# Performance work log

Hardware: AMD Instinct MI355X
Metric: run time of the kernel (lower is better)

Reference implementation:

```python
import jax, jax.numpy as jnp
import numpy as np
import math

B, H, S, F = 2, 16, 2048, 128

def setup_inputs() -> dict:
    key = jax.random.key(0)
    ks = jax.random.split(key, 7)
    scale = 1.0 / math.sqrt(F)
    x = jax.random.normal(ks[0], (B, H, S, F), dtype=jnp.float32)
    # torch nn.Linear weight is [out, in]; stacked per head -> [H, out, in]
    Wq = jax.random.uniform(ks[1], (H, F, F), jnp.float32, -scale, scale)
    Wk = jax.random.uniform(ks[2], (H, F, F), jnp.float32, -scale, scale)
    Wv = jax.random.uniform(ks[3], (H, F, F), jnp.float32, -scale, scale)
    bq = jax.random.uniform(ks[4], (H, F), jnp.float32, -scale, scale)
    bk = jax.random.uniform(ks[5], (H, F), jnp.float32, -scale, scale)
    bv = jax.random.uniform(ks[6], (H, F), jnp.float32, -scale, scale)
    return {"x": x, "Wq": Wq, "Wk": Wk, "Wv": Wv, "bq": bq, "bk": bk, "bv": bv}

def reference(x, Wq, Wk, Wv, bq, bk, bv):
    # Per-head linear projections (y = x @ W.T + b), batched over heads via einsum
    q = jnp.einsum('bhsf,hef->bhse', x, Wq) + bq[None, :, None, :]
    k = jnp.einsum('bhsf,hef->bhse', x, Wk) + bk[None, :, None, :]
    v = jnp.einsum('bhsf,hef->bhse', x, Wv) + bv[None, :, None, :]
    # Scores [B,H,S,S]
    scores = jnp.einsum('bhqe,bhke->bhqk', q, k)
    # Causal mask (strict upper triangle set to -inf) applied BEFORE scaling,
    # matching the original (dividing -inf by sqrt(F) keeps it -inf)
    causal = jnp.triu(jnp.ones((S, S), dtype=bool), k=1)
    scores = jnp.where(causal[None, None], -jnp.inf, scores)
    scores = scores / jnp.sqrt(jnp.float32(x.shape[-1]))
    weights = jax.nn.softmax(scores, axis=-1)
    return jnp.einsum('bhqk,bhke->bhqe', weights, v)
```

## Files before the change

kernel.cpp:

```cpp
#include <hip/hip_runtime.h>
#include <hip/hip_bf16.h>

#define SLEN 2048
#define FDIM 128
#define NH   16
#define NBH  32
#define QBLK 64
#define KVB  64
#define NQT  (SLEN / QBLK)

typedef __attribute__((ext_vector_type(8)))  __bf16 bf16x8;
typedef __attribute__((ext_vector_type(8)))  short  s16x8;
typedef __attribute__((ext_vector_type(4)))  short  s16x4;
typedef __attribute__((ext_vector_type(4)))  float  f32x4;
typedef __attribute__((ext_vector_type(16))) float  f32x16;
typedef __attribute__((ext_vector_type(4)))  int    i32x4;

__device__ __forceinline__ unsigned short f2bf_u(float f) {
    union { float f; unsigned u; } t;
    t.f = f;
    unsigned r = t.u + 0x7FFFu + ((t.u >> 16) & 1u);
    return (unsigned short)(r >> 16);
}
__device__ __forceinline__ short f2bf(float f) { return (short)f2bf_u(f); }
__device__ __forceinline__ unsigned pack2(float a, float b) {
    return (unsigned)f2bf_u(a) | ((unsigned)f2bf_u(b) << 16);
}

__device__ __forceinline__ float ex2(float x) {
    float r;
    asm volatile("v_exp_f32 %0, %1" : "=v"(r) : "v"(x));
    return r;
}

__device__ __forceinline__ void gld16(const void* g, void* l) {
    __builtin_amdgcn_global_load_lds(
        (const __attribute__((address_space(1))) void*)g,
        (__attribute__((address_space(3))) void*)l, 16, 0, 0);
}

__global__ __launch_bounds__(256, 2) void qkv_proj(
    const float* __restrict__ x,
    const float* __restrict__ Wq, const float* __restrict__ Wk, const float* __restrict__ Wv,
    const float* __restrict__ bq, const float* __restrict__ bk, const float* __restrict__ bv,
    short* __restrict__ Q, short* __restrict__ K, short* __restrict__ Vt)
{
    const int zi = blockIdx.z;
    const int bh = blockIdx.y;
    const int h  = bh & (NH - 1);
    const int st = blockIdx.x;

    const float* W    = (zi == 0) ? Wq : (zi == 1) ? Wk : Wv;
    const float* bias = (zi == 0) ? bq : (zi == 1) ? bk : bv;
    W    += (size_t)h * FDIM * FDIM;
    bias += h * FDIM;
    const float* xg = x + ((size_t)bh * SLEN + st * 64) * FDIM;

    __shared__ __align__(16) short lx[64][136];
    __shared__ __align__(16) short lw[128][136];

    const int t = threadIdx.x;
    {
        int r = t >> 4, c = (t & 15) * 8;
        #pragma unroll
        for (int it = 0; it < 4; ++it) {
            const float* src = &xg[(size_t)(r + it * 16) * FDIM + c];
            f32x4 a = *(const f32x4*)&src[0];
            f32x4 b = *(const f32x4*)&src[4];
            s16x8 o;
            #pragma unroll
            for (int j = 0; j < 4; ++j) { o[j] = f2bf(a[j]); o[4 + j] = f2bf(b[j]); }
            *(s16x8*)&lx[r + it * 16][c] = o;
        }
        #pragma unroll
        for (int it = 0; it < 8; ++it) {
            const float* src = &W[(size_t)(r + it * 16) * FDIM + c];
            f32x4 a = *(const f32x4*)&src[0];
            f32x4 b = *(const f32x4*)&src[4];
            s16x8 o;
            #pragma unroll
            for (int j = 0; j < 4; ++j) { o[j] = f2bf(a[j]); o[4 + j] = f2bf(b[j]); }
            *(s16x8*)&lw[r + it * 16][c] = o;
        }
    }
    __syncthreads();

    const int wid = t >> 6, lane = t & 63;
    const int wr = (wid >> 1) * 32;
    const int wc = (wid & 1) * 64;
    const int lr = lane & 15, lk = (lane >> 4) * 8, hi4 = (lane >> 4) * 4;

    f32x4 acc[2][4] = {};
    #pragma unroll
    for (int ks = 0; ks < 4; ++ks) {
        int kb = ks * 32 + lk;
        bf16x8 a[2], b[4];
        #pragma unroll
        for (int m = 0; m < 2; ++m) a[m] = *(const bf16x8*)&lx[wr + m * 16 + lr][kb];
        #pragma unroll
        for (int n = 0; n < 4; ++n) b[n] = *(const bf16x8*)&lw[wc + n * 16 + lr][kb];
        #pragma unroll
        for (int m = 0; m < 2; ++m)
            #pragma unroll
            for (int n = 0; n < 4; ++n)
                acc[m][n] = __builtin_amdgcn_mfma_f32_16x16x32_bf16(a[m], b[n], acc[m][n], 0, 0, 0);
    }

    if (zi == 0) {
        short* og = Q + ((size_t)bh * SLEN + st * 64) * FDIM;
        const float sc = 0.12751744526f;
        #pragma unroll
        for (int n = 0; n < 4; ++n) {
            int col = wc + n * 16 + lr;
            float bb = bias[col];
            #pragma unroll
            for (int m = 0; m < 2; ++m) {
                int r0 = wr + m * 16 + hi4;
                #pragma unroll
                for (int j = 0; j < 4; ++j)
                    og[(size_t)(r0 + j) * FDIM + col] = f2bf((acc[m][n][j] + bb) * sc);
            }
        }
    } else if (zi == 1) {
        short* og = K + (size_t)bh * SLEN * FDIM;
        #pragma unroll
        for (int n = 0; n < 4; ++n) {
            int col = wc + n * 16 + lr;
            float bb = bias[col];
            #pragma unroll
            for (int m = 0; m < 2; ++m) {
                int s0 = st * 64 + wr + m * 16 + hi4;
                #pragma unroll
                for (int j = 0; j < 4; ++j) {
                    int s = s0 + j;
                    int idx = (s * FDIM + col) ^ ((s & 15) << 3);
                    og[idx] = f2bf(acc[m][n][j] + bb);
                }
            }
        }
    } else {
        short* ogT = Vt + (size_t)bh * SLEN * FDIM;
        const int hp = (hi4 == 4) ? 8 : (hi4 == 8) ? 4 : hi4;
        #pragma unroll
        for (int n = 0; n < 4; ++n) {
            int col = wc + n * 16 + lr;
            float bb = bias[col];
            const int cb  = col >> 5, qlp = col & 31;
            #pragma unroll
            for (int m = 0; m < 2; ++m) {
                const int kb16 = wr + m * 16;
                const int hs_  = kb16 >> 5;
                const int s2_  = (kb16 >> 4) & 1;
                const int hi2_ = hp >> 3;
                const int j0   = hp & 7;
                s16x4 w;
                #pragma unroll
                for (int j = 0; j < 4; ++j) w[j] = f2bf(acc[m][n][j] + bb);
                size_t addr = (size_t)st * 8192 + hs_ * 4096 + cb * 1024
                            + s2_ * 512 + (hi2_ * 32 + qlp) * 8 + j0;
                *(s16x4*)&ogT[addr] = w;
            }
        }
    }
}

__global__ __launch_bounds__(256, 2) void attn_fwd(
    const short* __restrict__ Qg, const short* __restrict__ Kg,
    const short* __restrict__ vTg, float* __restrict__ out)
{
    __shared__ __align__(16) char smem[34816];
    float* obuf = (float*)smem;
    float* mlb  = (float*)(smem + 33792);

    const int bid = blockIdx.x;
    const int qt  = (NQT - 1) - (bid >> 5);
    const int bh  = bid & 31;

    const int t = threadIdx.x, wid = t >> 6, lane = t & 63;
    const int ql  = lane & 31;
    const int hi2 = lane >> 5;
    const int qb  = wid & 1;
    const int hs  = wid >> 1;
    const size_t base = (size_t)bh * SLEN * FDIM;

    const char*  kgb = (const char*)(Kg + base);
    const short* vgb = vTg + base + hs * 4096 + (size_t)lane * 8;

    bf16x8 qf[8];
    {
        const short* qp = Qg + base + (size_t)(qt * QBLK + qb * 32 + ql) * FDIM;
        #pragma unroll
        for (int ks = 0; ks < 8; ++ks) qf[ks] = *(const bf16x8*)&qp[ks * 16 + hi2 * 8];
    }

    f32x16 oacc[4] = {};
    float m_run = -1e30f, l_run = 0.f;

    #define STAGE(ktile, buf) do {                                               \
        const char* kt_ = kgb + (size_t)(ktile) * 16384;                         \
        _Pragma("unroll")                                                        \
        for (int i_ = 0; i_ < 4; ++i_)                                           \
            gld16(kt_ + wid * 4096 + i_ * 1024 + lane * 16,                      \
                  smem + (buf) * 16384 + wid * 4096 + i_ * 1024);                \
    } while (0)

    STAGE(0, 0);
    __syncthreads();

    const int nkt = qt + 1;
    int cur = 0;
    const int kswz = (ql & 15) << 3;

    for (int kt = 0; kt < nkt; ++kt) {
        bf16x8 vfr[8];
        {
            const short* vb_ = vgb + (size_t)kt * 8192;
            #pragma unroll
            for (int cb = 0; cb < 4; ++cb) {
                vfr[cb * 2 + 0] = *(const bf16x8*)&vb_[cb * 1024];
                vfr[cb * 2 + 1] = *(const bf16x8*)&vb_[cb * 1024 + 512];
            }
        }
        if (kt + 1 < nkt) STAGE(kt + 1, cur ^ 1);

        const char* kbuf = smem + cur * 16384;

        const int Rrow = hs * 32 + ql;
        f32x16 sfr = {};
        __builtin_amdgcn_s_setprio(1);
        #pragma unroll
        for (int ks = 0; ks < 8; ++ks) {
            bf16x8 kf = *(const bf16x8*)(kbuf + (size_t)(((Rrow * 128 + ks * 16 + hi2 * 8) ^ kswz) * 2));
            sfr = __builtin_amdgcn_mfma_f32_32x32x16_bf16(kf, qf[ks], sfr, 0, 0, 0);
        }
        __builtin_amdgcn_s_setprio(0);

        if (kt == qt) {
            if (hs > qb) {
                #pragma unroll
                for (int r = 0; r < 16; ++r) sfr[r] = -__builtin_inff();
            } else if (hs == qb) {
                #pragma unroll
                for (int r = 0; r < 16; ++r) {
                    int kl = (r & 3) + 8 * (r >> 2) + 4 * hi2;
                    if (kl > ql) sfr[r] = -__builtin_inff();
                }
            }
        }

        float a0 = fmaxf(fmaxf(sfr[0],  sfr[1]),  sfr[2]);
        float a1 = fmaxf(fmaxf(sfr[3],  sfr[4]),  sfr[5]);
        float a2 = fmaxf(fmaxf(sfr[6],  sfr[7]),  sfr[8]);
        float a3 = fmaxf(fmaxf(sfr[9],  sfr[10]), sfr[11]);
        float a4 = fmaxf(fmaxf(sfr[12], sfr[13]), sfr[14]);
        float b0 = fmaxf(fmaxf(a0, a1), a2);
        float b1 = fmaxf(fmaxf(a3, a4), sfr[15]);
        float rm = fmaxf(b0, b1);
        rm = fmaxf(rm, __shfl_xor(rm, 32));
        if (!__all(rm <= m_run)) {
            float mnew = fmaxf(m_run, rm);
            float fac  = ex2(m_run - mnew);
            l_run *= fac;
            #pragma unroll
            for (int cb = 0; cb < 4; ++cb) oacc[cb] *= fac;
            m_run = mnew;
        }
        float pe[16];
        #pragma unroll
        for (int r = 0; r < 16; ++r) pe[r] = ex2(sfr[r] - m_run);
        float s0 = (pe[0] + pe[1]) + (pe[2] + pe[3]);
        float s1 = (pe[4] + pe[5]) + (pe[6] + pe[7]);
        float s2 = (pe[8] + pe[9]) + (pe[10] + pe[11]);
        float s3 = (pe[12] + pe[13]) + (pe[14] + pe[15]);
        float ssum = (s0 + s1) + (s2 + s3);
        l_run += ssum + __shfl_xor(ssum, 32);

        bf16x8 pf[2];
        #pragma unroll
        for (int s2_ = 0; s2_ < 2; ++s2_) {
            const int b = s2_ * 8;
            union { unsigned u[4]; bf16x8 v; } w;
            w.u[0] = pack2(pe[b + 0], pe[b + 1]);
            w.u[1] = pack2(pe[b + 2], pe[b + 3]);
            w.u[2] = pack2(pe[b + 4], pe[b + 5]);
            w.u[3] = pack2(pe[b + 6], pe[b + 7]);
            pf[s2_] = w.v;
        }

        __builtin_amdgcn_s_setprio(1);
        #pragma unroll
        for (int cb = 0; cb < 4; ++cb) {
            #pragma unroll
            for (int s2_ = 0; s2_ < 2; ++s2_)
                oacc[cb] = __builtin_amdgcn_mfma_f32_32x32x16_bf16(vfr[cb * 2 + s2_], pf[s2_], oacc[cb], 0, 0, 0);
        }
        __builtin_amdgcn_s_setprio(0);

        __syncthreads();
        cur ^= 1;
    }
    #undef STAGE

    if (lane < 32) {
        mlb[(wid * 32 + ql) * 2 + 0] = m_run;
        mlb[(wid * 32 + ql) * 2 + 1] = l_run;
    }
    if (hs == 1) {
        #pragma unroll
        for (int cb = 0; cb < 4; ++cb)
            #pragma unroll
            for (int r = 0; r < 16; ++r) {
                int e = cb * 32 + (r & 3) + 8 * (r >> 2) + 4 * hi2;
                obuf[(qb * 32 + ql) * 132 + e] = oacc[cb][r];
            }
    }
    __syncthreads();
    if (hs == 0) {
        float m2 = mlb[((wid + 2) * 32 + ql) * 2 + 0];
        float l2 = mlb[((wid + 2) * 32 + ql) * 2 + 1];
        float M  = fmaxf(m_run, m2);
        float a  = ex2(m_run - M);
        float b2 = ex2(m2 - M);
        float inv = 1.f / (l_run * a + l2 * b2);
        float* orow = out + base + (size_t)(qt * QBLK + qb * 32 + ql) * FDIM;
        #pragma unroll
        for (int cb = 0; cb < 4; ++cb)
            #pragma unroll
            for (int r = 0; r < 16; ++r) {
                int e = cb * 32 + (r & 3) + 8 * (r >> 2) + 4 * hi2;
                orow[e] = (oacc[cb][r] * a + obuf[(qb * 32 + ql) * 132 + e] * b2) * inv;
            }
    }
}

extern "C" void kernel_launch(void* const* d_in, const int* in_sizes, int n_in,
                              void* d_out, int out_size, void* d_ws, size_t ws_size,
                              hipStream_t stream) {
    (void)in_sizes; (void)n_in; (void)out_size; (void)ws_size;
    const float* x  = (const float*)d_in[0];
    const float* Wq = (const float*)d_in[1];
    const float* Wk = (const float*)d_in[2];
    const float* Wv = (const float*)d_in[3];
    const float* bq = (const float*)d_in[4];
    const float* bk = (const float*)d_in[5];
    const float* bv = (const float*)d_in[6];

    const size_t elems = (size_t)NBH * SLEN * FDIM;
    short* Q  = (short*)d_ws;
    short* K  = Q + elems;
    short* Vt = K + elems;

    qkv_proj<<<dim3(SLEN / 64, NBH, 3), 256, 0, stream>>>(x, Wq, Wk, Wv, bq, bk, bv, Q, K, Vt);
    attn_fwd<<<dim3(NQT * NBH), 256, 0, stream>>>(Q, K, Vt, (float*)d_out);
}
```

Baseline: 93.30 us.

## Fuse QKV projections per tile, pre-convert weights, reorder attention tiles

```diff
diff --git a/kernel.cpp b/kernel.cpp
--- a/kernel.cpp
+++ b/kernel.cpp
@@ -23,8 +23,11 @@
     return (unsigned short)(r >> 16);
 }
 __device__ __forceinline__ short f2bf(float f) { return (short)f2bf_u(f); }
-__device__ __forceinline__ unsigned pack2(float a, float b) {
-    return (unsigned)f2bf_u(a) | ((unsigned)f2bf_u(b) << 16);
+
+__device__ __forceinline__ unsigned cvt_pk_bf16(float lo, float hi) {
+    unsigned r;
+    asm("v_cvt_pk_bf16_f32 %0, %1, %2" : "=v"(r) : "v"(lo), "v"(hi));
+    return r;
 }
 
 __device__ __forceinline__ float ex2(float x) {
@@ -39,27 +42,56 @@
         (__attribute__((address_space(3))) void*)l, 16, 0, 0);
 }
 
-__global__ __launch_bounds__(256, 2) void qkv_proj(
-    const float* __restrict__ x,
-    const float* __restrict__ Wq, const float* __restrict__ Wk, const float* __restrict__ Wv,
+__global__ __launch_bounds__(256, 4) void wconv(
+    const float* __restrict__ Wq, const float* __restrict__ Wk,
+    const float* __restrict__ Wv, short* __restrict__ Wb)
+{
+    const int bid = blockIdx.x;
+    const int z = bid >> 6, rem = bid & 63;
+    const int h = rem >> 2, qd = rem & 3;
+    const float* Wm = ((z == 0) ? Wq : (z == 1) ? Wk : Wv) + (size_t)h * 16384;
+    short* O = Wb + ((size_t)z * NH + h) * 16384;
+    const int t = threadIdx.x;
+    #pragma unroll
+    for (int it = 0; it < 2; ++it) {
+        int idx = qd * 4096 + it * 2048 + t * 8;
+        int e = idx >> 7, c = idx & 127;
+        f32x4 a = *(const f32x4*)&Wm[idx];
+        f32x4 b = *(const f32x4*)&Wm[idx + 4];
+        union { unsigned u[4]; s16x8 v; } o;
+        o.u[0] = cvt_pk_bf16(a[0], a[1]);
+        o.u[1] = cvt_pk_bf16(a[2], a[3]);
+        o.u[2] = cvt_pk_bf16(b[0], b[1]);
+        o.u[3] = cvt_pk_bf16(b[2], b[3]);
+        *(s16x8*)&O[(e << 7) | (c ^ ((e & 15) << 3))] = o.v;
+    }
+}
+
+__global__ __launch_bounds__(256, 2) void qkv_fused(
+    const float* __restrict__ x, const short* __restrict__ Wb,
     const float* __restrict__ bq, const float* __restrict__ bk, const float* __restrict__ bv,
     short* __restrict__ Q, short* __restrict__ K, short* __restrict__ Vt)
 {
-    const int zi = blockIdx.z;
     const int bh = blockIdx.y;
     const int h  = bh & (NH - 1);
     const int st = blockIdx.x;
-
-    const float* W    = (zi == 0) ? Wq : (zi == 1) ? Wk : Wv;
-    const float* bias = (zi == 0) ? bq : (zi == 1) ? bk : bv;
-    W    += (size_t)h * FDIM * FDIM;
-    bias += h * FDIM;
     const float* xg = x + ((size_t)bh * SLEN + st * 64) * FDIM;
 
     __shared__ __align__(16) short lx[64][136];
-    __shared__ __align__(16) short lw[128][136];
+    __shared__ __align__(16) short lw[128][128];
 
     const int t = threadIdx.x;
+    const int wid = t >> 6, lane = t & 63;
+
+    #define WSTAGE(zz) do {                                                     \
+        const char* wsrc_ = (const char*)(Wb + ((size_t)(zz) * NH + h) * 16384);\
+        _Pragma("unroll")                                                       \
+        for (int i_ = 0; i_ < 8; ++i_)                                          \
+            gld16(wsrc_ + wid * 8192 + i_ * 1024 + lane * 16,                   \
+                  (char*)&lw[0][0] + wid * 8192 + i_ * 1024);                   \
+    } while (0)
+
+    WSTAGE(0);
     {
         int r = t >> 4, c = (t & 15) * 8;
         #pragma unroll
@@ -67,101 +99,102 @@
             const float* src = &xg[(size_t)(r + it * 16) * FDIM + c];
             f32x4 a = *(const f32x4*)&src[0];
             f32x4 b = *(const f32x4*)&src[4];
-            s16x8 o;
-            #pragma unroll
-            for (int j = 0; j < 4; ++j) { o[j] = f2bf(a[j]); o[4 + j] = f2bf(b[j]); }
-            *(s16x8*)&lx[r + it * 16][c] = o;
-        }
-        #pragma unroll
-        for (int it = 0; it < 8; ++it) {
-            const float* src = &W[(size_t)(r + it * 16) * FDIM + c];
-            f32x4 a = *(const f32x4*)&src[0];
-            f32x4 b = *(const f32x4*)&src[4];
-            s16x8 o;
-            #pragma unroll
-            for (int j = 0; j < 4; ++j) { o[j] = f2bf(a[j]); o[4 + j] = f2bf(b[j]); }
-            *(s16x8*)&lw[r + it * 16][c] = o;
+            union { unsigned u[4]; s16x8 v; } o;
+            o.u[0] = cvt_pk_bf16(a[0], a[1]);
+            o.u[1] = cvt_pk_bf16(a[2], a[3]);
+            o.u[2] = cvt_pk_bf16(b[0], b[1]);
+            o.u[3] = cvt_pk_bf16(b[2], b[3]);
+            *(s16x8*)&lx[r + it * 16][c] = o.v;
         }
     }
     __syncthreads();
 
-    const int wid = t >> 6, lane = t & 63;
     const int wr = (wid >> 1) * 32;
     const int wc = (wid & 1) * 64;
     const int lr = lane & 15, lk = (lane >> 4) * 8, hi4 = (lane >> 4) * 4;
-
-    f32x4 acc[2][4] = {};
+    const short* lwp = &lw[0][0];
+    const int swz = lr << 3;
+
     #pragma unroll
-    for (int ks = 0; ks < 4; ++ks) {
-        int kb = ks * 32 + lk;
-        bf16x8 a[2], b[4];
-        #pragma unroll
-        for (int m = 0; m < 2; ++m) a[m] = *(const bf16x8*)&lx[wr + m * 16 + lr][kb];
-        #pragma unroll
-        for (int n = 0; n < 4; ++n) b[n] = *(const bf16x8*)&lw[wc + n * 16 + lr][kb];
-        #pragma unroll
-        for (int m = 0; m < 2; ++m)
+    for (int z = 0; z < 3; ++z) {
+        f32x4 acc[2][4] = {};
+        #pragma unroll
+        for (int ks = 0; ks < 4; ++ks) {
+            int kb = ks * 32 + lk;
+            bf16x8 a[2], b[4];
+            #pragma unroll
+            for (int m = 0; m < 2; ++m) a[m] = *(const bf16x8*)&lx[wr + m * 16 + lr][kb];
             #pragma unroll
             for (int n = 0; n < 4; ++n)
-                acc[m][n] = __builtin_amdgcn_mfma_f32_16x16x32_bf16(a[m], b[n], acc[m][n], 0, 0, 0);
-    }
-
-    if (zi == 0) {
-        short* og = Q + ((size_t)bh * SLEN + st * 64) * FDIM;
-        const float sc = 0.12751744526f;
-        #pragma unroll
-        for (int n = 0; n < 4; ++n) {
-            int col = wc + n * 16 + lr;
-            float bb = bias[col];
-            #pragma unroll
-            for (int m = 0; m < 2; ++m) {
-                int r0 = wr + m * 16 + hi4;
-                #pragma unroll
-                for (int j = 0; j < 4; ++j)
-                    og[(size_t)(r0 + j) * FDIM + col] = f2bf((acc[m][n][j] + bb) * sc);
-            }
-        }
-    } else if (zi == 1) {
-        short* og = K + (size_t)bh * SLEN * FDIM;
-        #pragma unroll
-        for (int n = 0; n < 4; ++n) {
-            int col = wc + n * 16 + lr;
-            float bb = bias[col];
-            #pragma unroll
-            for (int m = 0; m < 2; ++m) {
-                int s0 = st * 64 + wr + m * 16 + hi4;
-                #pragma unroll
-                for (int j = 0; j < 4; ++j) {
-                    int s = s0 + j;
-                    int idx = (s * FDIM + col) ^ ((s & 15) << 3);
-                    og[idx] = f2bf(acc[m][n][j] + bb);
+                b[n] = *(const bf16x8*)&lwp[(size_t)(wc + n * 16 + lr) * 128 + (kb ^ swz)];
+            #pragma unroll
+            for (int m = 0; m < 2; ++m)
+                #pragma unroll
+                for (int n = 0; n < 4; ++n)
+                    acc[m][n] = __builtin_amdgcn_mfma_f32_16x16x32_bf16(a[m], b[n], acc[m][n], 0, 0, 0);
+        }
+        if (z < 2) { __syncthreads(); WSTAGE(z + 1); }
+
+        const float* bias = ((z == 0) ? bq : (z == 1) ? bk : bv) + h * FDIM;
+        if (z == 0) {
+            short* og = Q + ((size_t)bh * SLEN + st * 64) * FDIM;
+            const float sc = 0.12751744526f;
+            #pragma unroll
+            for (int n = 0; n < 4; ++n) {
+                int col = wc + n * 16 + lr;
+                float bb = bias[col];
+                #pragma unroll
+                for (int m = 0; m < 2; ++m) {
+                    int r0 = wr + m * 16 + hi4;
+                    #pragma unroll
+                    for (int j = 0; j < 4; ++j)
+                        og[(size_t)(r0 + j) * FDIM + col] = f2bf((acc[m][n][j] + bb) * sc);
                 }
             }
-        }
-    } else {
-        short* ogT = Vt + (size_t)bh * SLEN * FDIM;
-        const int hp = (hi4 == 4) ? 8 : (hi4 == 8) ? 4 : hi4;
-        #pragma unroll
-        for (int n = 0; n < 4; ++n) {
-            int col = wc + n * 16 + lr;
-            float bb = bias[col];
-            const int cb  = col >> 5, qlp = col & 31;
-            #pragma unroll
-            for (int m = 0; m < 2; ++m) {
-                const int kb16 = wr + m * 16;
-                const int hs_  = kb16 >> 5;
-                const int s2_  = (kb16 >> 4) & 1;
-                const int hi2_ = hp >> 3;
-                const int j0   = hp & 7;
-                s16x4 w;
-                #pragma unroll
-                for (int j = 0; j < 4; ++j) w[j] = f2bf(acc[m][n][j] + bb);
-                size_t addr = (size_t)st * 8192 + hs_ * 4096 + cb * 1024
-                            + s2_ * 512 + (hi2_ * 32 + qlp) * 8 + j0;
-                *(s16x4*)&ogT[addr] = w;
-            }
-        }
-    }
+        } else if (z == 1) {
+            short* og = K + (size_t)bh * SLEN * FDIM;
+            #pragma unroll
+            for (int n = 0; n < 4; ++n) {
+                int col = wc + n * 16 + lr;
+                float bb = bias[col];
+                #pragma unroll
+                for (int m = 0; m < 2; ++m) {
+                    int s0 = st * 64 + wr + m * 16 + hi4;
+                    #pragma unroll
+                    for (int j = 0; j < 4; ++j) {
+                        int s = s0 + j;
+                        int idx = (s * FDIM + col) ^ ((s & 15) << 3);
+                        og[idx] = f2bf(acc[m][n][j] + bb);
+                    }
+                }
+            }
+        } else {
+            short* ogT = Vt + (size_t)bh * SLEN * FDIM;
+            const int hp = (hi4 == 4) ? 8 : (hi4 == 8) ? 4 : hi4;
+            #pragma unroll
+            for (int n = 0; n < 4; ++n) {
+                int col = wc + n * 16 + lr;
+                float bb = bias[col];
+                const int cb  = col >> 5, qlp = col & 31;
+                #pragma unroll
+                for (int m = 0; m < 2; ++m) {
+                    const int kb16 = wr + m * 16;
+                    const int hs_  = kb16 >> 5;
+                    const int s2_  = (kb16 >> 4) & 1;
+                    const int hi2_ = hp >> 3;
+                    const int j0   = hp & 7;
+                    union { unsigned u[2]; s16x4 v; } w;
+                    w.u[0] = cvt_pk_bf16(acc[m][n][0] + bb, acc[m][n][1] + bb);
+                    w.u[1] = cvt_pk_bf16(acc[m][n][2] + bb, acc[m][n][3] + bb);
+                    size_t addr = (size_t)st * 8192 + hs_ * 4096 + cb * 1024
+                                + s2_ * 512 + (hi2_ * 32 + qlp) * 8 + j0;
+                    *(s16x4*)&ogT[addr] = w.v;
+                }
+            }
+        }
+        if (z < 2) __syncthreads();
+    }
+    #undef WSTAGE
 }
 
 __global__ __launch_bounds__(256, 2) void attn_fwd(
@@ -173,8 +206,11 @@
     float* mlb  = (float*)(smem + 33792);
 
     const int bid = blockIdx.x;
-    const int qt  = (NQT - 1) - (bid >> 5);
     const int bh  = bid & 31;
+    const int i   = ((bid >> 5) & 7) + ((bid >> 8) << 3);
+    const int grp = i >> 3, k = i & 7;
+    const int qt  = (grp == 0) ? (31 - k) : (grp == 1) ? (8 + k)
+                  : (grp == 2) ? (23 - k) : k;
 
     const int t = threadIdx.x, wid = t >> 6, lane = t & 63;
     const int ql  = lane & 31;
@@ -257,7 +293,7 @@
         float b1 = fmaxf(fmaxf(a3, a4), sfr[15]);
         float rm = fmaxf(b0, b1);
         rm = fmaxf(rm, __shfl_xor(rm, 32));
-        if (!__all(rm <= m_run)) {
+        if (!__all(rm <= m_run + 8.f)) {
             float mnew = fmaxf(m_run, rm);
             float fac  = ex2(m_run - mnew);
             l_run *= fac;
@@ -280,10 +316,10 @@
         for (int s2_ = 0; s2_ < 2; ++s2_) {
             const int b = s2_ * 8;
             union { unsigned u[4]; bf16x8 v; } w;
-            w.u[0] = pack2(pe[b + 0], pe[b + 1]);
-            w.u[1] = pack2(pe[b + 2], pe[b + 3]);
-            w.u[2] = pack2(pe[b + 4], pe[b + 5]);
-            w.u[3] = pack2(pe[b + 6], pe[b + 7]);
+            w.u[0] = cvt_pk_bf16(pe[b + 0], pe[b + 1]);
+            w.u[1] = cvt_pk_bf16(pe[b + 2], pe[b + 3]);
+            w.u[2] = cvt_pk_bf16(pe[b + 4], pe[b + 5]);
+            w.u[3] = cvt_pk_bf16(pe[b + 6], pe[b + 7]);
             pf[s2_] = w.v;
         }
 
@@ -336,7 +372,7 @@
 extern "C" void kernel_launch(void* const* d_in, const int* in_sizes, int n_in,
                               void* d_out, int out_size, void* d_ws, size_t ws_size,
                               hipStream_t stream) {
-    (void)in_sizes; (void)n_in; (void)out_size; (void)ws_size;
+    (void)in_sizes; (void)n_in; (void)out_size;
     const float* x  = (const float*)d_in[0];
     const float* Wq = (const float*)d_in[1];
     const float* Wk = (const float*)d_in[2];
@@ -346,10 +382,14 @@
     const float* bv = (const float*)d_in[6];
 
     const size_t elems = (size_t)NBH * SLEN * FDIM;
+    const size_t wb_shorts = (size_t)3 * NH * FDIM * FDIM;
     short* Q  = (short*)d_ws;
     short* K  = Q + elems;
     short* Vt = K + elems;
-
-    qkv_proj<<<dim3(SLEN / 64, NBH, 3), 256, 0, stream>>>(x, Wq, Wk, Wv, bq, bk, bv, Q, K, Vt);
+    short* Wb = (ws_size >= (3 * elems + wb_shorts) * sizeof(short))
+              ? (Vt + elems) : (short*)d_out;
+
+    wconv<<<dim3(192), 256, 0, stream>>>(Wq, Wk, Wv, Wb);
+    qkv_fused<<<dim3(SLEN / 64, NBH), 256, 0, stream>>>(x, Wb, bq, bk, bv, Q, K, Vt);
     attn_fwd<<<dim3(NQT * NBH), 256, 0, stream>>>(Q, K, Vt, (float*)d_out);
 }
```

After: 81.35 us. -12.8%, faster.
